# Optimization experiments

Hardware: AMD Instinct MI355X
Metric: run time of the kernel (lower is better)

The kernel has to match this reference:

```python
import jax, jax.numpy as jnp
import numpy as np

N_USERS = 100000
N_ITEMS = 200000
NNZ = 5000000
DIM = 64
N_LAYERS = 3
ALPHA = 0.5


def setup_inputs() -> dict:
    key = jax.random.key(0)
    ks = jax.random.split(key, 9)
    N = N_USERS + N_ITEMS
    users = jax.random.randint(ks[0], (4096,), 0, N_USERS, dtype=jnp.int64 if jax.config.jax_enable_x64 else jnp.int32)
    items = jax.random.randint(ks[1], (4096,), 0, N_ITEMS, dtype=users.dtype)
    rows = jax.random.randint(ks[2], (NNZ,), 0, N, dtype=users.dtype)
    cols = jax.random.randint(ks[3], (NNZ,), 0, N, dtype=users.dtype)
    vals = jax.random.uniform(ks[4], (NNZ,), dtype=jnp.float32)
    user_emb = jax.random.normal(ks[5], (N_USERS, DIM), dtype=jnp.float32)
    item_emb = jax.random.normal(ks[6], (N_ITEMS, DIM), dtype=jnp.float32)
    user_emb0 = jax.random.normal(ks[7], (N_USERS, DIM), dtype=jnp.float32)
    item_emb0 = jax.random.normal(ks[8], (N_ITEMS, DIM), dtype=jnp.float32)
    return {"users": users, "items": items, "rows": rows, "cols": cols,
            "vals": vals, "user_emb": user_emb, "item_emb": item_emb,
            "user_emb0": user_emb0, "item_emb0": item_emb0}


def _computer(vals, user_emb, item_emb, user_emb0, item_emb0, rows, cols):
    # LightGCN propagation with scaled SVD residual (VS_LightGCN.computer)
    N = user_emb.shape[0] + item_emb.shape[0]
    all_emb = jnp.concatenate([user_emb, item_emb], axis=0)      # [N, D]
    all_emb0 = jnp.concatenate([user_emb0, item_emb0], axis=0)   # [N, D]
    embs = [all_emb]
    for layer in range(N_LAYERS):
        # SpMM: out[r] = sum_{e: rows[e]==r} vals[e] * all_emb[cols[e]]
        msg = vals[:, None] * all_emb[cols]                      # [nnz, D]
        all_emb = jax.ops.segment_sum(msg, rows, num_segments=N) + ALPHA * all_emb0
        embs.append((N_LAYERS - layer) * all_emb)
    light_out = jnp.mean(jnp.stack(embs, axis=1), axis=1)        # [N, D]
    return light_out


def reference(users, items, rows, cols, vals, user_emb, item_emb, user_emb0, item_emb0):
    light_out = _computer(vals, user_emb, item_emb, user_emb0, item_emb0, rows, cols)
    users_emb = light_out[users]                                 # [B, D]
    items_emb = light_out[user_emb.shape[0] + items]             # [B, D]
    gamma = jnp.sum(users_emb * items_emb, axis=1)               # [B]
    return gamma
```

## Files before the change

### kernel.cpp

```cpp
#include <hip/hip_runtime.h>

#define ALPHA 0.5f
#define BSHIFT 11
#define RPB 2048
#define MAXB 256
#define PCHUNK 16384


__device__ __forceinline__ float bf2f(unsigned short u) {
  return __uint_as_float((unsigned)u << 16);
}
__device__ __forceinline__ unsigned short f2bf(float f) {
  unsigned u = __float_as_uint(f);
  u += 0x7fffu + ((u >> 16) & 1u);
  return (unsigned short)(u >> 16);
}


__global__ __launch_bounds__(256) void k_count(
    const int* __restrict__ rows, int nnz, int* __restrict__ bcnt) {
  __shared__ int lcnt[MAXB];
  int t = threadIdx.x;
  if (t < MAXB) lcnt[t] = 0;
  __syncthreads();
  int stride = 512 * 256;
  for (int e = blockIdx.x * 256 + t; e < nnz; e += stride)
    atomicAdd(&lcnt[rows[e] >> BSHIFT], 1);
  __syncthreads();
  if (t < MAXB) {
    int c = lcnt[t];
    if (c) atomicAdd(&bcnt[t], c);
  }
}


__global__ void k_scan_buckets(const int* __restrict__ bcnt, int nb,
                               int* __restrict__ bptr, int* __restrict__ bcur) {
  __shared__ int s[256];
  int t = threadIdx.x;
  int v = (t < nb) ? bcnt[t] : 0;
  s[t] = v; __syncthreads();
  for (int d = 1; d < 256; d <<= 1) {
    int x = (t >= d) ? s[t - d] : 0;
    __syncthreads();
    s[t] += x;
    __syncthreads();
  }
  if (t < nb) {
    int excl = s[t] - v;
    bptr[t] = excl;
    bcur[t] = excl;
  }
  if (t == 0) bptr[nb] = s[255];
}


__global__ __launch_bounds__(1024) void k_part_conv(
    const int* __restrict__ rows, const int* __restrict__ cols, const float* __restrict__ vals,
    int nnz, int* __restrict__ bcur, uint2* __restrict__ pPay, int PB,
    const float* __restrict__ uE, const float* __restrict__ iE,
    int nU64, int nTot, unsigned short* __restrict__ out) {
  __shared__ int lcnt[MAXB];
  __shared__ int lbase[MAXB];
  int t = threadIdx.x;
  if ((int)blockIdx.x < PB) {
    if (t < MAXB) lcnt[t] = 0;
    __syncthreads();
    int base = blockIdx.x * PCHUNK;
    int end = nnz < base + PCHUNK ? nnz : base + PCHUNK;
    for (int e = base + t; e < end; e += 1024)
      atomicAdd(&lcnt[rows[e] >> BSHIFT], 1);
    __syncthreads();
    if (t < MAXB) {
      int c = lcnt[t];
      lbase[t] = c ? atomicAdd(&bcur[t], c) : 0;
      lcnt[t] = 0;
    }
    __syncthreads();
    for (int e = base + t; e < end; e += 1024) {
      int r = rows[e];
      int b = r >> BSHIFT;
      int p = lbase[b] + atomicAdd(&lcnt[b], 1);
      uint2 pay;
      pay.x = ((unsigned)(r & (RPB - 1)) << 20) | (unsigned)cols[e];
      pay.y = __float_as_uint(vals[e]);
      pPay[p] = pay;
    }
  } else {
    int i = (((int)blockIdx.x - PB) * 1024 + t) * 4;
    if (i >= nTot) return;
    const float* src = (i < nU64) ? (uE + i) : (iE + (i - nU64));
    float4 v = *(const float4*)src;
    ushort4 o;
    o.x = f2bf(v.x); o.y = f2bf(v.y); o.z = f2bf(v.z); o.w = f2bf(v.w);
    *(ushort4*)(out + i) = o;
  }
}


__global__ __launch_bounds__(1024) void k_build_csr(
    const int* __restrict__ bptr, const uint2* __restrict__ pPay, int N,
    int* __restrict__ rowptr, int* __restrict__ cnt, int2* __restrict__ colval,
    int* __restrict__ degHist) {
  __shared__ int lcnt[RPB];
  __shared__ int scanbuf[1024];
  __shared__ int ldeg[256];
  int t = threadIdx.x;
  int b = blockIdx.x;
  int r0 = b << BSHIFT;
  int rCount = N - r0; if (rCount > RPB) rCount = RPB;
  int eBeg = bptr[b], eEnd = bptr[b + 1];

  for (int r = t; r < RPB; r += 1024) lcnt[r] = 0;
  if (t < 256) ldeg[t] = 0;
  __syncthreads();
  for (int e = eBeg + t; e < eEnd; e += 1024)
    atomicAdd(&lcnt[pPay[e].x >> 20], 1);
  __syncthreads();
  for (int r = t; r < rCount; r += 1024) {
    int c = lcnt[r];
    cnt[r0 + r] = c;
    atomicAdd(&ldeg[c < 255 ? c : 255], 1);
  }
  int v2[2]; int s = 0;
#pragma unroll
  for (int k = 0; k < 2; k++) {
    int x = lcnt[2 * t + k];
    v2[k] = s; s += x;
  }
  scanbuf[t] = s; __syncthreads();
  for (int d = 1; d < 1024; d <<= 1) {
    int x = (t >= d) ? scanbuf[t - d] : 0;
    __syncthreads();
    scanbuf[t] += x;
    __syncthreads();
  }
  int blockExcl = scanbuf[t] - s;
#pragma unroll
  for (int k = 0; k < 2; k++) lcnt[2 * t + k] = blockExcl + v2[k];
  __syncthreads();
  if (t < 256 && ldeg[t]) atomicAdd(&degHist[t], ldeg[t]);
  for (int r = t; r < rCount; r += 1024) rowptr[r0 + r] = eBeg + lcnt[r];
  __syncthreads();
  for (int e = eBeg + t; e < eEnd; e += 1024) {
    uint2 pay = pPay[e];
    int r = (int)(pay.x >> 20);
    int p = eBeg + atomicAdd(&lcnt[r], 1);
    int2 cv; cv.x = (int)(pay.x & 0xFFFFFu); cv.y = (int)pay.y;
    colval[p] = cv;
  }
}


__global__ void k_degscan(const int* __restrict__ degHist, int* __restrict__ degCur,
                          int2* __restrict__ colval, int nnz) {
  __shared__ int s[256];
  int t = threadIdx.x;
  int v = degHist[t];
  s[t] = v; __syncthreads();
  for (int d = 1; d < 256; d <<= 1) {
    int x = (t >= d) ? s[t - d] : 0;
    __syncthreads();
    s[t] += x;
    __syncthreads();
  }
  degCur[t] = s[t] - v;
  if (t < 8) { int2 z; z.x = 0; z.y = 0; colval[nnz + t] = z; }
}


__global__ __launch_bounds__(256) void k_permute(
    const int* __restrict__ rowptr, const int* __restrict__ cnt, int N,
    int* __restrict__ degCur,
    int* __restrict__ perm, int* __restrict__ rowptrS, int* __restrict__ lenS) {
  __shared__ int lcnt[256];
  __shared__ int lbase[256];
  int t = threadIdx.x;
  lcnt[t] = 0;
  __syncthreads();
  int base = blockIdx.x * 1024;
  int end = N < base + 1024 ? N : base + 1024;
  for (int r = base + t; r < end; r += 256) {
    int c = cnt[r];
    atomicAdd(&lcnt[c < 255 ? c : 255], 1);
  }
  __syncthreads();
  {
    int c = lcnt[t];
    lbase[t] = c ? atomicAdd(&degCur[t], c) : 0;
    lcnt[t] = 0;
  }
  __syncthreads();
  for (int r = base + t; r < end; r += 256) {
    int c = cnt[r];
    int bin = c < 255 ? c : 255;
    int pos = lbase[bin] + atomicAdd(&lcnt[bin], 1);
    perm[pos] = r;
    rowptrS[pos] = rowptr[r];
    lenS[pos] = c;
  }
}


__device__ __forceinline__ void spmm_body(
    int gtid,
    const unsigned short* __restrict__ src,
    const float* __restrict__ e0U, const float* __restrict__ e0I, int split,
    const int* __restrict__ perm, const int* __restrict__ rowptrS, const int* __restrict__ lenS,
    const int2* __restrict__ colval,
    unsigned short* __restrict__ dst, int n) {
  int wave = gtid >> 6;
  int lane = gtid & 63;
  int sub = lane >> 4;
  int k   = lane & 15;
  int q = wave * 4 + sub;
  int s0 = 2 * q, s1 = 2 * q + 1;
  bool va = s0 < n, vb = s1 < n;
  int i0 = va ? s0 : 0, i1 = vb ? s1 : 0;
  int row0 = perm[i0], row1 = perm[i1];
  int st0 = rowptrS[i0], st1 = rowptrS[i1];
  int len0 = va ? lenS[i0] : 0, len1 = vb ? lenS[i1] : 0;
  const int2* cv0 = colval + st0;
  const int2* cv1 = colval + st1;
  const unsigned short* srcK = src + (size_t)k * 4;
  int l0m = len0 > 0 ? len0 - 1 : 0;
  int l1m = len1 > 0 ? len1 - 1 : 0;
  int mx = max(len0, len1);

  float p0 = 0.f, p1 = 0.f, p2 = 0.f, p3 = 0.f;
  float r0a = 0.f, r1a = 0.f, r2a = 0.f, r3a = 0.f;
  for (int j = 0; j < mx; j += 2) {
    int ja = j, jb = j + 1;
    int j0a = ja < l0m ? ja : l0m, j0b = jb < l0m ? jb : l0m;
    int j1a = ja < l1m ? ja : l1m, j1b = jb < l1m ? jb : l1m;
    int2 e0a = cv0[j0a];
    int2 e0b = cv0[j0b];
    int2 e1a = cv1[j1a];
    int2 e1b = cv1[j1b];
    ushort4 x0a = *(const ushort4*)(srcK + (size_t)e0a.x * 64);
    ushort4 x0b = *(const ushort4*)(srcK + (size_t)e0b.x * 64);
    ushort4 x1a = *(const ushort4*)(srcK + (size_t)e1a.x * 64);
    ushort4 x1b = *(const ushort4*)(srcK + (size_t)e1b.x * 64);
    float w0a = ja < len0 ? __int_as_float(e0a.y) : 0.f;
    float w0b = jb < len0 ? __int_as_float(e0b.y) : 0.f;
    float w1a = ja < len1 ? __int_as_float(e1a.y) : 0.f;
    float w1b = jb < len1 ? __int_as_float(e1b.y) : 0.f;
    p0 = fmaf(w0a, bf2f(x0a.x), p0); p1 = fmaf(w0a, bf2f(x0a.y), p1);
    p2 = fmaf(w0a, bf2f(x0a.z), p2); p3 = fmaf(w0a, bf2f(x0a.w), p3);
    p0 = fmaf(w0b, bf2f(x0b.x), p0); p1 = fmaf(w0b, bf2f(x0b.y), p1);
    p2 = fmaf(w0b, bf2f(x0b.z), p2); p3 = fmaf(w0b, bf2f(x0b.w), p3);
    r0a = fmaf(w1a, bf2f(x1a.x), r0a); r1a = fmaf(w1a, bf2f(x1a.y), r1a);
    r2a = fmaf(w1a, bf2f(x1a.z), r2a); r3a = fmaf(w1a, bf2f(x1a.w), r3a);
    r0a = fmaf(w1b, bf2f(x1b.x), r0a); r1a = fmaf(w1b, bf2f(x1b.y), r1a);
    r2a = fmaf(w1b, bf2f(x1b.z), r2a); r3a = fmaf(w1b, bf2f(x1b.w), r3a);
  }
  if (va) {
    const float* e0p = (row0 < split) ? (e0U + (size_t)row0 * 64)
                                      : (e0I + (size_t)(row0 - split) * 64);
    float4 ev = *(const float4*)(e0p + k * 4);
    ushort4 o;
    o.x = f2bf(p0 + ALPHA * ev.x);
    o.y = f2bf(p1 + ALPHA * ev.y);
    o.z = f2bf(p2 + ALPHA * ev.z);
    o.w = f2bf(p3 + ALPHA * ev.w);
    *(ushort4*)(dst + (size_t)row0 * 64 + k * 4) = o;
  }
  if (vb) {
    const float* e0p = (row1 < split) ? (e0U + (size_t)row1 * 64)
                                      : (e0I + (size_t)(row1 - split) * 64);
    float4 ev = *(const float4*)(e0p + k * 4);
    ushort4 o;
    o.x = f2bf(r0a + ALPHA * ev.x);
    o.y = f2bf(r1a + ALPHA * ev.y);
    o.z = f2bf(r2a + ALPHA * ev.z);
    o.w = f2bf(r3a + ALPHA * ev.w);
    *(ushort4*)(dst + (size_t)row1 * 64 + k * 4) = o;
  }
}

__global__ __launch_bounds__(256) void k_spmm(
    const unsigned short* __restrict__ src,
    const float* __restrict__ e0U, const float* __restrict__ e0I, int split,
    const int* __restrict__ perm, const int* __restrict__ rowptrS, const int* __restrict__ lenS,
    const int2* __restrict__ colval,
    unsigned short* __restrict__ dst, int n) {
  spmm_body((int)(blockIdx.x * 256 + threadIdx.x), src, e0U, e0I, split,
            perm, rowptrS, lenS, colval, dst, n);
}

__global__ __launch_bounds__(256) void k_spmm2_acc(
    const unsigned short* __restrict__ ebA,
    const float* __restrict__ e0U, const float* __restrict__ e0I, int split,
    const int* __restrict__ perm, const int* __restrict__ rowptrS, const int* __restrict__ lenS,
    const int2* __restrict__ colval,
    unsigned short* __restrict__ ebB, int n, int spmmBlocks,
    const int* __restrict__ users, const int* __restrict__ items, int B,
    const float* __restrict__ user_emb, const float* __restrict__ item_emb,
    float* __restrict__ accU, float* __restrict__ accI) {
  if ((int)blockIdx.x < spmmBlocks) {
    spmm_body((int)(blockIdx.x * 256 + threadIdx.x), ebA, e0U, e0I, split,
              perm, rowptrS, lenS, colval, ebB, n);
  } else {
    int t = ((int)blockIdx.x - spmmBlocks) * 256 + threadIdx.x;
    int total = B * 64;
    if (t < total) {
      int b = t >> 6, d = t & 63;
      size_t idx = (size_t)users[b] * 64 + d;
      accU[t] = user_emb[idx] + 3.f * bf2f(ebA[idx]);
    } else if (t < 2 * total) {
      int t2 = t - total;
      int b = t2 >> 6, d = t2 & 63;
      int r = items[b];
      accI[t2] = item_emb[(size_t)r * 64 + d] + 3.f * bf2f(ebA[(size_t)(split + r) * 64 + d]);
    }
  }
}


__global__ __launch_bounds__(256) void k_mini3(
    const int* __restrict__ users, const int* __restrict__ items, int B, int split,
    const unsigned short* __restrict__ ebB,
    const float* __restrict__ e0U, const float* __restrict__ e0I,
    const int* __restrict__ rowptr, const int* __restrict__ cnt,
    const int2* __restrict__ colval,
    float* __restrict__ accU, float* __restrict__ accI) {
  int wave = (int)((blockIdx.x * blockDim.x + threadIdx.x) >> 6);
  int lane = threadIdx.x & 63;
  int sub = lane >> 4;
  int k   = lane & 15;
  int idx = wave * 4 + sub;
  bool valid = idx < 2 * B;
  int ic = valid ? idx : 0;
  int row;
  float* accp;
  if (ic < B) { row = users[ic];             accp = accU + (size_t)ic * 64; }
  else        { row = split + items[ic - B]; accp = accI + (size_t)(ic - B) * 64; }
  int start = rowptr[row];
  int len   = valid ? cnt[row] : 0;
  int maxlen = len;
  maxlen = max(maxlen, __shfl_xor(maxlen, 16));
  maxlen = max(maxlen, __shfl_xor(maxlen, 32));
  const int2* cv = colval + start;
  const unsigned short* srcK = ebB + (size_t)k * 4;
  int lenm1 = (len > 0) ? (len - 1) : 0;

  float a0 = 0.f, a1 = 0.f, a2 = 0.f, a3 = 0.f;
  for (int j = 0; j < maxlen; j += 4) {
#pragma unroll
    for (int u = 0; u < 4; u++) {
      int jj = j + u;
      int jc = (jj < len) ? jj : lenm1;
      int2 e = cv[jc];
      float v = (jj < len) ? __int_as_float(e.y) : 0.f;
      ushort4 x = *(const ushort4*)(srcK + (size_t)e.x * 64);
      a0 = fmaf(v, bf2f(x.x), a0);
      a1 = fmaf(v, bf2f(x.y), a1);
      a2 = fmaf(v, bf2f(x.z), a2);
      a3 = fmaf(v, bf2f(x.w), a3);
    }
  }
  if (valid) {
    const float* e0p = (row < split) ? (e0U + (size_t)row * 64)
                                     : (e0I + (size_t)(row - split) * 64);
    float4 ev = *(const float4*)(e0p + k * 4);
    ushort4 x2 = *(const ushort4*)(srcK + (size_t)row * 64);
    float4 cur = *(const float4*)(accp + k * 4);
    cur.x += a0 + ALPHA * ev.x + 2.f * bf2f(x2.x);
    cur.y += a1 + ALPHA * ev.y + 2.f * bf2f(x2.y);
    cur.z += a2 + ALPHA * ev.z + 2.f * bf2f(x2.z);
    cur.w += a3 + ALPHA * ev.w + 2.f * bf2f(x2.w);
    *(float4*)(accp + k * 4) = cur;
  }
}

__global__ void k_dot(const float* __restrict__ accU, const float* __restrict__ accI, int B,
                      float* __restrict__ out) {
  int wave = (int)((blockIdx.x * blockDim.x + threadIdx.x) >> 6);
  int lane = threadIdx.x & 63;
  if (wave >= B) return;
  float p = accU[(size_t)wave * 64 + lane] * accI[(size_t)wave * 64 + lane];
  for (int d = 32; d > 0; d >>= 1) p += __shfl_xor(p, d);
  if (lane == 0) out[wave] = p * (1.f / 16.f);
}


extern "C" void kernel_launch(void* const* d_in, const int* in_sizes, int n_in,
                              void* d_out, int out_size, void* d_ws, size_t ws_size,
                              hipStream_t stream) {
  const int*   users     = (const int*)d_in[0];
  const int*   items     = (const int*)d_in[1];
  const int*   rows      = (const int*)d_in[2];
  const int*   cols      = (const int*)d_in[3];
  const float* vals      = (const float*)d_in[4];
  const float* user_emb  = (const float*)d_in[5];
  const float* item_emb  = (const float*)d_in[6];
  const float* user_emb0 = (const float*)d_in[7];
  const float* item_emb0 = (const float*)d_in[8];
  float* gamma = (float*)d_out;

  int B   = in_sizes[0];
  int nnz = in_sizes[2];
  int nU  = in_sizes[5] / 64;
  int nI  = in_sizes[6] / 64;
  int N   = nU + nI;
  int nb  = (N + RPB - 1) >> BSHIFT;

  char* base = (char*)d_ws;
  unsigned short* ebIn = (unsigned short*)base;
  unsigned short* ebA  = ebIn + (size_t)N * 64;
  unsigned short* ebB  = ebA  + (size_t)N * 64;
  uint2* pPay = (uint2*)ebA;
  char* p = (char*)(ebB + (size_t)N * 64);
  int2* colval  = (int2*)p;           p += ((size_t)nnz + 8) * sizeof(int2);
  int*  rowptr  = (int*)p;            p += (size_t)N * sizeof(int);
  int*  cnt     = (int*)p;            p += (size_t)N * sizeof(int);
  int*  perm    = (int*)p;            p += (size_t)N * sizeof(int);
  int*  rowptrS = (int*)p;            p += (size_t)N * sizeof(int);
  int*  lenS    = (int*)p;            p += (size_t)N * sizeof(int);
  int*  bcnt    = (int*)p;            p += MAXB * sizeof(int);
  int*  degHist = (int*)p;            p += 256 * sizeof(int);
  int*  bptr    = (int*)p;            p += (MAXB + 1) * sizeof(int);
  int*  bcur    = (int*)p;            p += MAXB * sizeof(int);
  int*  degCur  = (int*)p;            p += 256 * sizeof(int);
  float* accU   = (float*)p;          p += (size_t)B * 64 * sizeof(float);
  float* accI   = (float*)p;          p += (size_t)B * 64 * sizeof(float);

  hipMemsetAsync(bcnt, 0, (MAXB + 256) * sizeof(int), stream);

  const int tpb = 256;
  int nTot = N * 64;

  k_count<<<512, tpb, 0, stream>>>(rows, nnz, bcnt);
  k_scan_buckets<<<1, 256, 0, stream>>>(bcnt, nb, bptr, bcur);

  int PB = (nnz + PCHUNK - 1) / PCHUNK;
  int convB = (nTot / 4 + 1023) / 1024;
  k_part_conv<<<PB + convB, 1024, 0, stream>>>(rows, cols, vals, nnz, bcur, pPay, PB,
                                               user_emb, item_emb, nU * 64, nTot, ebIn);

  k_build_csr<<<nb, 1024, 0, stream>>>(bptr, pPay, N, rowptr, cnt, colval, degHist);
  k_degscan<<<1, 256, 0, stream>>>(degHist, degCur, colval, nnz);
  k_permute<<<(N + 1023) / 1024, tpb, 0, stream>>>(rowptr, cnt, N, degCur, perm, rowptrS, lenS);

  int spmmBlocks = (N + 31) / 32;
  int accBlocks = (2 * B * 64 + tpb - 1) / tpb;

  k_spmm<<<spmmBlocks, tpb, 0, stream>>>(ebIn, user_emb0, item_emb0, nU,
                                         perm, rowptrS, lenS, colval, ebA, N);

  k_spmm2_acc<<<spmmBlocks + accBlocks, tpb, 0, stream>>>(ebA, user_emb0, item_emb0, nU,
                                                          perm, rowptrS, lenS, colval, ebB, N,
                                                          spmmBlocks, users, items, B,
                                                          user_emb, item_emb, accU, accI);

  int mBlocks = (2 * B + 15) / 16;
  k_mini3<<<mBlocks, tpb, 0, stream>>>(users, items, B, nU, ebB,
                                       user_emb0, item_emb0,
                                       rowptr, cnt, colval, accU, accI);

  k_dot<<<(B * 64 + tpb - 1) / tpb, tpb, 0, stream>>>(accU, accI, B, gamma);
}
```

Measured before the change: 615.6 us.

## Compute second SpMM layer only for rows needed by final query neighborhoods

Marks the queried user and item rows and their direct neighbors, then compacts the degree-sorted row list down to those rows. The second propagation layer runs only over that subset, since layer three is evaluated only for the query rows. This adds a marking pass, a compaction kernel and a larger memset in exchange for skipping most of one full SpMM. The mini3 inner loop also switches from clamped loads to a guarded branch. With about 8k query rows and an average degree near 17, the marked set is still a sizable fraction of N.

```diff
diff --git a/kernel.cpp b/kernel.cpp
--- a/kernel.cpp
+++ b/kernel.cpp
@@ -278,28 +278,81 @@
   }
 }
 
-__global__ __launch_bounds__(256) void k_spmm(
+
+__global__ __launch_bounds__(256) void k_spmm1_mark(
     const unsigned short* __restrict__ src,
     const float* __restrict__ e0U, const float* __restrict__ e0I, int split,
     const int* __restrict__ perm, const int* __restrict__ rowptrS, const int* __restrict__ lenS,
     const int2* __restrict__ colval,
-    unsigned short* __restrict__ dst, int n) {
-  spmm_body((int)(blockIdx.x * 256 + threadIdx.x), src, e0U, e0I, split,
-            perm, rowptrS, lenS, colval, dst, n);
+    unsigned short* __restrict__ dst, int n, int MB,
+    const int* __restrict__ users, const int* __restrict__ items, int B,
+    const int* __restrict__ rowptr, const int* __restrict__ cnt,
+    unsigned char* __restrict__ flag) {
+  if ((int)blockIdx.x < MB) {
+    int t = (int)blockIdx.x * 256 + threadIdx.x;
+    int wave = t >> 6;
+    int lane = t & 63;
+    int sub = lane >> 4;
+    int k = lane & 15;
+    int idx = wave * 4 + sub;
+    if (idx >= 2 * B) return;
+    int row = (idx < B) ? users[idx] : split + items[idx - B];
+    if (k == 0) flag[row] = 1;
+    int start = rowptr[row], len = cnt[row];
+    for (int j = k; j < len; j += 16) flag[colval[start + j].x] = 1;
+  } else {
+    spmm_body((int)((blockIdx.x - MB) * 256 + threadIdx.x), src, e0U, e0I, split,
+              perm, rowptrS, lenS, colval, dst, n);
+  }
+}
+
+
+__global__ __launch_bounds__(1024) void k_compact(
+    const int* __restrict__ perm, const int* __restrict__ rowptrS, const int* __restrict__ lenS,
+    const unsigned char* __restrict__ flag, int N, int* __restrict__ selTotal,
+    int* __restrict__ selPerm, int* __restrict__ selRowptrS, int* __restrict__ selLenS) {
+  __shared__ int sbuf[1024];
+  __shared__ int sbase;
+  int t = threadIdx.x;
+  int i = (int)blockIdx.x * 1024 + t;
+  int f = 0, r = 0, rp = 0, ln = 0;
+  if (i < N) {
+    r = perm[i];
+    f = flag[r];
+    if (f) { rp = rowptrS[i]; ln = lenS[i]; }
+  }
+  sbuf[t] = f; __syncthreads();
+  for (int d = 1; d < 1024; d <<= 1) {
+    int x = (t >= d) ? sbuf[t - d] : 0;
+    __syncthreads();
+    sbuf[t] += x;
+    __syncthreads();
+  }
+  int incl = sbuf[t];
+  if (t == 1023) sbase = atomicAdd(selTotal, incl);
+  __syncthreads();
+  if (f) {
+    int pos = sbase + incl - 1;
+    selPerm[pos] = r;
+    selRowptrS[pos] = rp;
+    selLenS[pos] = ln;
+  }
 }
 
 __global__ __launch_bounds__(256) void k_spmm2_acc(
     const unsigned short* __restrict__ ebA,
     const float* __restrict__ e0U, const float* __restrict__ e0I, int split,
-    const int* __restrict__ perm, const int* __restrict__ rowptrS, const int* __restrict__ lenS,
+    const int* __restrict__ selPerm, const int* __restrict__ selRowptrS,
+    const int* __restrict__ selLenS, const int* __restrict__ nSelPtr,
     const int2* __restrict__ colval,
-    unsigned short* __restrict__ ebB, int n, int spmmBlocks,
+    unsigned short* __restrict__ ebB, int spmmBlocks,
     const int* __restrict__ users, const int* __restrict__ items, int B,
     const float* __restrict__ user_emb, const float* __restrict__ item_emb,
     float* __restrict__ accU, float* __restrict__ accI) {
   if ((int)blockIdx.x < spmmBlocks) {
+    int nSel = *nSelPtr;
     spmm_body((int)(blockIdx.x * 256 + threadIdx.x), ebA, e0U, e0I, split,
-              perm, rowptrS, lenS, colval, ebB, n);
+              selPerm, selRowptrS, selLenS, colval, ebB, nSel);
   } else {
     int t = ((int)blockIdx.x - spmmBlocks) * 256 + threadIdx.x;
     int total = B * 64;
@@ -342,21 +395,21 @@
   maxlen = max(maxlen, __shfl_xor(maxlen, 32));
   const int2* cv = colval + start;
   const unsigned short* srcK = ebB + (size_t)k * 4;
-  int lenm1 = (len > 0) ? (len - 1) : 0;
 
   float a0 = 0.f, a1 = 0.f, a2 = 0.f, a3 = 0.f;
   for (int j = 0; j < maxlen; j += 4) {
 #pragma unroll
     for (int u = 0; u < 4; u++) {
       int jj = j + u;
-      int jc = (jj < len) ? jj : lenm1;
-      int2 e = cv[jc];
-      float v = (jj < len) ? __int_as_float(e.y) : 0.f;
-      ushort4 x = *(const ushort4*)(srcK + (size_t)e.x * 64);
-      a0 = fmaf(v, bf2f(x.x), a0);
-      a1 = fmaf(v, bf2f(x.y), a1);
-      a2 = fmaf(v, bf2f(x.z), a2);
-      a3 = fmaf(v, bf2f(x.w), a3);
+      if (jj < len) {
+        int2 e = cv[jj];
+        float v = __int_as_float(e.y);
+        ushort4 x = *(const ushort4*)(srcK + (size_t)e.x * 64);
+        a0 = fmaf(v, bf2f(x.x), a0);
+        a1 = fmaf(v, bf2f(x.y), a1);
+        a2 = fmaf(v, bf2f(x.z), a2);
+        a3 = fmaf(v, bf2f(x.w), a3);
+      }
     }
   }
   if (valid) {
@@ -404,6 +457,7 @@
   int nI  = in_sizes[6] / 64;
   int N   = nU + nI;
   int nb  = (N + RPB - 1) >> BSHIFT;
+  int Nf  = (N + 15) & ~15;
 
   char* base = (char*)d_ws;
   unsigned short* ebIn = (unsigned short*)base;
@@ -417,15 +471,20 @@
   int*  perm    = (int*)p;            p += (size_t)N * sizeof(int);
   int*  rowptrS = (int*)p;            p += (size_t)N * sizeof(int);
   int*  lenS    = (int*)p;            p += (size_t)N * sizeof(int);
+  int*  selPerm    = (int*)p;         p += (size_t)N * sizeof(int);
+  int*  selRowptrS = (int*)p;         p += (size_t)N * sizeof(int);
+  int*  selLenS    = (int*)p;         p += (size_t)N * sizeof(int);
   int*  bcnt    = (int*)p;            p += MAXB * sizeof(int);
   int*  degHist = (int*)p;            p += 256 * sizeof(int);
+  int*  selTotal= (int*)p;            p += 4 * sizeof(int);
+  unsigned char* flag = (unsigned char*)p; p += Nf;
   int*  bptr    = (int*)p;            p += (MAXB + 1) * sizeof(int);
   int*  bcur    = (int*)p;            p += MAXB * sizeof(int);
   int*  degCur  = (int*)p;            p += 256 * sizeof(int);
   float* accU   = (float*)p;          p += (size_t)B * 64 * sizeof(float);
   float* accI   = (float*)p;          p += (size_t)B * 64 * sizeof(float);
 
-  hipMemsetAsync(bcnt, 0, (MAXB + 256) * sizeof(int), stream);
+  hipMemsetAsync(bcnt, 0, (MAXB + 256 + 4) * sizeof(int) + Nf, stream);
 
   const int tpb = 256;
   int nTot = N * 64;
@@ -444,14 +503,18 @@
 
   int spmmBlocks = (N + 31) / 32;
   int accBlocks = (2 * B * 64 + tpb - 1) / tpb;
-
-  k_spmm<<<spmmBlocks, tpb, 0, stream>>>(ebIn, user_emb0, item_emb0, nU,
-                                         perm, rowptrS, lenS, colval, ebA, N);
-
-  k_spmm2_acc<<<spmmBlocks + accBlocks, tpb, 0, stream>>>(ebA, user_emb0, item_emb0, nU,
-                                                          perm, rowptrS, lenS, colval, ebB, N,
-                                                          spmmBlocks, users, items, B,
-                                                          user_emb, item_emb, accU, accI);
+  int markBlocks = (2 * B + 15) / 16;
+
+  k_spmm1_mark<<<markBlocks + spmmBlocks, tpb, 0, stream>>>(
+      ebIn, user_emb0, item_emb0, nU, perm, rowptrS, lenS, colval, ebA, N,
+      markBlocks, users, items, B, rowptr, cnt, flag);
+
+  k_compact<<<(N + 1023) / 1024, 1024, 0, stream>>>(perm, rowptrS, lenS, flag, N,
+                                                    selTotal, selPerm, selRowptrS, selLenS);
+
+  k_spmm2_acc<<<spmmBlocks + accBlocks, tpb, 0, stream>>>(
+      ebA, user_emb0, item_emb0, nU, selPerm, selRowptrS, selLenS, selTotal,
+      colval, ebB, spmmBlocks, users, items, B, user_emb, item_emb, accU, accI);
 
   int mBlocks = (2 * B + 15) / 16;
   k_mini3<<<mBlocks, tpb, 0, stream>>>(users, items, B, nU, ebB,
```

Result: faster. 564.6 us (-8.3%).
